# Kernel tuning notes

Hardware: AMD Instinct MI355X
Metric: run time of the kernel (lower is better)

The kernel has to match this reference:

```python
import jax, jax.numpy as jnp
import numpy as np

B, C_IN, C_OUT, N_VERT, K = 8, 64, 64, 40962, 7


def setup_inputs() -> dict:
    key = jax.random.key(0)
    k1, k2, k3, k4 = jax.random.split(key, 4)
    x = jax.random.normal(k1, (B, C_IN, N_VERT), dtype=jnp.float32)
    neigh_indices = jax.random.randint(k2, (N_VERT, K), 0, N_VERT, dtype=jnp.int64)
    # nn.Linear(in=K*C_IN, out=C_OUT): weight [C_OUT, K*C_IN], bias [C_OUT]
    W = jax.random.normal(k3, (C_OUT, C_IN * K), dtype=jnp.float32) * (1.0 / np.sqrt(C_IN * K))
    b = jax.random.normal(k4, (C_OUT,), dtype=jnp.float32) * 0.01
    return {"x": x, "neigh_indices": neigh_indices, "W": W, "b": b}


def reference(x, neigh_indices, W, b):
    # x: [B, C_in, N]; neigh_indices: [N, K]
    # gather neighbor features: [B, C_in, N, K]
    gathered = x[:, :, neigh_indices]
    # Linear over flattened (C_in, K) per vertex. The torch flatten order is
    # (c, k) since mat is [B, N, C_in, K] reshaped to [B*N, C_in*K].
    Wr = W.reshape(W.shape[0], x.shape[1], neigh_indices.shape[1])  # [C_out, C_in, K]
    out = jnp.einsum('bcnk,ock->bon', gathered, Wr) + b[None, :, None]
    return out  # [B, C_out, N]
```

## Files before the change

### kernel.cpp

```cpp
#include <hip/hip_runtime.h>

#define BB 8
#define CI 64
#define CO 64
#define NV 40962
#define KN 7
#define KKD 448

typedef unsigned short u16;
typedef unsigned int u32;

typedef __bf16 bf16x8 __attribute__((ext_vector_type(8)));
typedef float f32x16 __attribute__((ext_vector_type(16)));

__device__ inline u16 f2bf(float f) {
    u32 u = __builtin_bit_cast(u32, f);
    u32 r = (u + 0x7FFFu + ((u >> 16) & 1u)) >> 16;
    return (u16)r;
}

__device__ inline void gload_lds16(const void* g, void* l) {
    __builtin_amdgcn_global_load_lds(
        (const __attribute__((address_space(1))) u32*)g,
        (__attribute__((address_space(3))) u32*)l, 16, 0, 0);
}

__global__ void transpose_x(const float* __restrict__ x, u16* __restrict__ xT) {
    __shared__ u16 tile[64][72];
    const int b = blockIdx.y;
    const int n0 = blockIdx.x * 64;
    const int tid = threadIdx.x;

#pragma unroll
    for (int i = 0; i < 16; ++i) {
        int flat = i * 256 + tid;
        int c = flat >> 6;
        int nn = flat & 63;
        int n = n0 + nn;
        if (n < NV) {
            float v = __builtin_nontemporal_load(&x[((size_t)b * CI + c) * NV + n]);
            tile[nn][c] = f2bf(v);
        }
    }
    __syncthreads();

#pragma unroll
    for (int i = 0; i < 2; ++i) {
        int flat8 = i * 256 + tid;
        int nn = flat8 >> 3;
        int c0 = (flat8 & 7) * 8;
        int n = n0 + nn;
        if (n < NV) {
            uint4 v = *(const uint4*)&tile[nn][c0];
            *(uint4*)&xT[((size_t)b * NV + n) * CI + c0] = v;
        }
    }
}

__global__ void pack_w(const float* __restrict__ W, u16* __restrict__ Wf) {
    int e = blockIdx.x * 256 + threadIdx.x;
    if (e < 2 * 28 * 64 * 8) {
        int j = e & 7;
        int lane = (e >> 3) & 63;
        int sg = e >> 9;
        int s = sg % 28;
        int rg = sg / 28;
        int o = rg * 32 + (lane & 31);
        int kk = s * 16 + ((lane >> 5) << 3) + j;
        int kn = kk >> 6;
        int c = kk & 63;
        Wf[e] = f2bf(W[o * KKD + c * KN + kn]);
    }
}

__global__ __launch_bounds__(256, 6) void conv_mfma(
    const u16* __restrict__ xT, const u16* __restrict__ Wf,
    const int* __restrict__ idx, const float* __restrict__ bias,
    float* __restrict__ out) {
    __shared__ alignas(16) u16 G[3][4096];

    const int bid = blockIdx.x;
    const int b = bid & 7;
    const int n0 = (bid >> 3) * 64;
    const int t = threadIdx.x;
    const int lane = t & 63;
    const int w = t >> 6;
    const int rg = w & 1;
    const int cg = w >> 1;
    const int col = lane & 31;
    const int half = lane >> 5;

    const char* xbc = (const char*)(xT + (size_t)b * NV * CI);
    const char* wfc = (const char*)Wf;

    const int sr0 = t >> 3;
    const int q = t & 7;
    const int qe = q ^ (sr0 & 7);

    int g0 = n0 + sr0;        if (g0 >= NV) g0 = NV - 1;
    int g1 = n0 + 32 + sr0;   if (g1 >= NV) g1 = NV - 1;

    int j0[KN], j1[KN];
    {
        int4 lo0 = *(const int4*)(idx + (size_t)g0 * KN);
        int4 hi0 = *(const int4*)(idx + (size_t)g0 * KN + 3);
        int4 lo1 = *(const int4*)(idx + (size_t)g1 * KN);
        int4 hi1 = *(const int4*)(idx + (size_t)g1 * KN + 3);
        j0[0] = lo0.x; j0[1] = lo0.y; j0[2] = lo0.z; j0[3] = lo0.w;
        j0[4] = hi0.y; j0[5] = hi0.z; j0[6] = hi0.w;
        j1[0] = lo1.x; j1[1] = lo1.y; j1[2] = lo1.z; j1[3] = lo1.w;
        j1[4] = hi1.y; j1[5] = hi1.z; j1[6] = hi1.w;
    }

    char* gb = (char*)&G[0][0];
    const u32 dst0 = (u32)(w * 1024);
    const u32 dst1 = (u32)(4096 + w * 1024);

    const int brow = cg * 32 + col;
    const u32 rbase = (u32)(brow * 128);
    const u32 rmask = (u32)(brow & 7) << 4;

    const u32 abase = (u32)((rg * 28) * 1024 + lane * 16);

    f32x16 acc{};

    gload_lds16(xbc + (size_t)j0[0] * 128 + qe * 16, gb + 0 * 8192 + dst0);
    gload_lds16(xbc + (size_t)j1[0] * 128 + qe * 16, gb + 0 * 8192 + dst1);
    __builtin_amdgcn_sched_barrier(0);
    uint4 acur0 = *(const uint4*)(wfc + abase + 0 * 1024);
    uint4 acur1 = *(const uint4*)(wfc + abase + 1 * 1024);
    uint4 acur2 = *(const uint4*)(wfc + abase + 2 * 1024);
    uint4 acur3 = *(const uint4*)(wfc + abase + 3 * 1024);
    __builtin_amdgcn_sched_barrier(0);
    gload_lds16(xbc + (size_t)j0[1] * 128 + qe * 16, gb + 1 * 8192 + dst0);
    gload_lds16(xbc + (size_t)j1[1] * 128 + qe * 16, gb + 1 * 8192 + dst1);
    __builtin_amdgcn_sched_barrier(0);

#pragma unroll
    for (int k = 0; k < KN; ++k) {
        uint4 an0, an1, an2, an3;
        if (k + 1 < KN) {
            u32 ab = abase + (u32)((k + 1) * 4 * 1024);
            an0 = *(const uint4*)(wfc + ab + 0 * 1024);
            an1 = *(const uint4*)(wfc + ab + 1 * 1024);
            an2 = *(const uint4*)(wfc + ab + 2 * 1024);
            an3 = *(const uint4*)(wfc + ab + 3 * 1024);
        }
        __builtin_amdgcn_sched_barrier(0);

        if (k <= 5) asm volatile("s_waitcnt vmcnt(6)" ::: "memory");
        else        asm volatile("s_waitcnt vmcnt(0)" ::: "memory");
        __builtin_amdgcn_sched_barrier(0);
        __builtin_amdgcn_s_barrier();
        __builtin_amdgcn_sched_barrier(0);

        if (k + 2 < KN) {
            u32 db = (u32)(((k + 2) % 3) * 8192);
            gload_lds16(xbc + (size_t)j0[k + 2] * 128 + qe * 16, gb + db + dst0);
            gload_lds16(xbc + (size_t)j1[k + 2] * 128 + qe * 16, gb + db + dst1);
        }
        __builtin_amdgcn_sched_barrier(0);

        const char* gsrc = gb + (u32)((k % 3) * 8192);
#pragma unroll
        for (int sub = 0; sub < 4; ++sub) {
            u32 boff = rbase + ((((u32)sub * 32) + (u32)half * 16) ^ rmask);
            uint4 bf = *(const uint4*)(gsrc + boff);
            uint4 af = (sub == 0) ? acur0 : (sub == 1) ? acur1 : (sub == 2) ? acur2 : acur3;
            acc = __builtin_amdgcn_mfma_f32_32x32x16_bf16(
                __builtin_bit_cast(bf16x8, af),
                __builtin_bit_cast(bf16x8, bf), acc, 0, 0, 0);
        }

        if (k + 1 < KN) { acur0 = an0; acur1 = an1; acur2 = an2; acur3 = an3; }
    }

    const int v = n0 + cg * 32 + col;
    if (v < NV) {
        float* ob = out + (size_t)b * CO * NV + v;
#pragma unroll
        for (int r = 0; r < 16; ++r) {
            int rowo = (r & 3) + 8 * (r >> 2) + 4 * half;
            int o = rg * 32 + rowo;
            ob[(size_t)o * NV] = acc[r] + bias[o];
        }
    }
}

__global__ void naive_conv(const float* __restrict__ x, const int* __restrict__ idx,
                           const float* __restrict__ W, const float* __restrict__ bias,
                           float* __restrict__ out) {
    const int b = blockIdx.y;
    const int n = blockIdx.x * 4 + (threadIdx.x & 3);
    const int o = threadIdx.x >> 2;
    if (n >= NV) return;
    float acc = bias[o];
    const float* xb = x + (size_t)b * CI * NV;
    const float* wo = W + o * KKD;
    for (int k = 0; k < KN; ++k) {
        int j = idx[n * KN + k];
        for (int c = 0; c < CI; ++c)
            acc += xb[(size_t)c * NV + j] * wo[c * KN + k];
    }
    out[((size_t)b * CO + o) * NV + n] = acc;
}

extern "C" void kernel_launch(void* const* d_in, const int* in_sizes, int n_in,
                              void* d_out, int out_size, void* d_ws, size_t ws_size,
                              hipStream_t stream) {
    const float* x    = (const float*)d_in[0];
    const int*   idx  = (const int*)d_in[1];
    const float* W    = (const float*)d_in[2];
    const float* bias = (const float*)d_in[3];
    float* out = (float*)d_out;

    const size_t xT_bytes = (size_t)BB * NV * CI * 2;
    const size_t wf_bytes = (size_t)2 * 28 * 64 * 8 * 2;
    const size_t need = xT_bytes + wf_bytes;

    if (ws_size >= need) {
        u16* xT = (u16*)d_ws;
        u16* Wf = (u16*)((char*)d_ws + xT_bytes);
        transpose_x<<<dim3((NV + 63) / 64, BB), 256, 0, stream>>>(x, xT);
        pack_w<<<dim3(112), 256, 0, stream>>>(W, Wf);
        const int ntiles = (NV + 63) / 64;
        conv_mfma<<<dim3(ntiles * BB), 256, 0, stream>>>(xT, Wf, idx, bias, out);
    } else {
        naive_conv<<<dim3((NV + 3) / 4, BB), 256, 0, stream>>>(x, idx, W, bias, out);
    }
}
```

Before: 79.34 us.

## Make conv kernel persistent with register-resident weights and cross-tile gather prefetch

The MFMA conv kernel becomes persistent: a grid of 512 blocks loops over vertex tiles with a stride of 64 tiles. Each wave loads its full packed weight slice into registers once and caches the bias. The 3-slot LDS ring now runs across tile boundaries, so gathers for the next tile's first neighbours and its index loads are issued during the current tile's compute. The aim is to remove per-block setup, reloading of weights, and the pipeline drain at tile ends. The cost is heavier register use and lower occupancy (launch bounds 2), and only 512 blocks may underfill the GPU's compute units.

```diff
diff --git a/kernel.cpp b/kernel.cpp
--- a/kernel.cpp
+++ b/kernel.cpp
@@ -6,12 +6,16 @@
 #define NV 40962
 #define KN 7
 #define KKD 448
+#define NTILES 641
+#define BPB 64
 
 typedef unsigned short u16;
 typedef unsigned int u32;
 
 typedef __bf16 bf16x8 __attribute__((ext_vector_type(8)));
 typedef float f32x16 __attribute__((ext_vector_type(16)));
+
+#define WAITV(N) asm volatile("s_waitcnt vmcnt(" #N ")" ::: "memory")
 
 __device__ inline u16 f2bf(float f) {
     u32 u = __builtin_bit_cast(u32, f);
@@ -73,7 +77,7 @@
     }
 }
 
-__global__ __launch_bounds__(256, 6) void conv_mfma(
+__global__ __launch_bounds__(256, 2) void conv_mfma(
     const u16* __restrict__ xT, const u16* __restrict__ Wf,
     const int* __restrict__ idx, const float* __restrict__ bias,
     float* __restrict__ out) {
@@ -81,7 +85,7 @@
 
     const int bid = blockIdx.x;
     const int b = bid & 7;
-    const int n0 = (bid >> 3) * 64;
+    const int tile0 = bid >> 3;
     const int t = threadIdx.x;
     const int lane = t & 63;
     const int w = t >> 6;
@@ -92,27 +96,11 @@
 
     const char* xbc = (const char*)(xT + (size_t)b * NV * CI);
     const char* wfc = (const char*)Wf;
+    char* gb = (char*)&G[0][0];
 
     const int sr0 = t >> 3;
     const int q = t & 7;
-    const int qe = q ^ (sr0 & 7);
-
-    int g0 = n0 + sr0;        if (g0 >= NV) g0 = NV - 1;
-    int g1 = n0 + 32 + sr0;   if (g1 >= NV) g1 = NV - 1;
-
-    int j0[KN], j1[KN];
-    {
-        int4 lo0 = *(const int4*)(idx + (size_t)g0 * KN);
-        int4 hi0 = *(const int4*)(idx + (size_t)g0 * KN + 3);
-        int4 lo1 = *(const int4*)(idx + (size_t)g1 * KN);
-        int4 hi1 = *(const int4*)(idx + (size_t)g1 * KN + 3);
-        j0[0] = lo0.x; j0[1] = lo0.y; j0[2] = lo0.z; j0[3] = lo0.w;
-        j0[4] = hi0.y; j0[5] = hi0.z; j0[6] = hi0.w;
-        j1[0] = lo1.x; j1[1] = lo1.y; j1[2] = lo1.z; j1[3] = lo1.w;
-        j1[4] = hi1.y; j1[5] = hi1.z; j1[6] = hi1.w;
-    }
-
-    char* gb = (char*)&G[0][0];
+    const u32 qe16 = (u32)((q ^ (sr0 & 7)) << 4);
     const u32 dst0 = (u32)(w * 1024);
     const u32 dst1 = (u32)(4096 + w * 1024);
 
@@ -120,70 +108,118 @@
     const u32 rbase = (u32)(brow * 128);
     const u32 rmask = (u32)(brow & 7) << 4;
 
-    const u32 abase = (u32)((rg * 28) * 1024 + lane * 16);
-
-    f32x16 acc{};
-
-    gload_lds16(xbc + (size_t)j0[0] * 128 + qe * 16, gb + 0 * 8192 + dst0);
-    gload_lds16(xbc + (size_t)j1[0] * 128 + qe * 16, gb + 0 * 8192 + dst1);
+    int jc0[KN], jc1[KN], jn0[KN], jn1[KN];
+    {
+        int nn0 = tile0 * 64 + sr0;      if (nn0 >= NV) nn0 = NV - 1;
+        int nn1 = tile0 * 64 + 32 + sr0; if (nn1 >= NV) nn1 = NV - 1;
+        int4 lo0 = *(const int4*)(idx + (size_t)nn0 * KN);
+        int4 hi0 = *(const int4*)(idx + (size_t)nn0 * KN + 3);
+        int4 lo1 = *(const int4*)(idx + (size_t)nn1 * KN);
+        int4 hi1 = *(const int4*)(idx + (size_t)nn1 * KN + 3);
+        jc0[0]=lo0.x; jc0[1]=lo0.y; jc0[2]=lo0.z; jc0[3]=lo0.w;
+        jc0[4]=hi0.y; jc0[5]=hi0.z; jc0[6]=hi0.w;
+        jc1[0]=lo1.x; jc1[1]=lo1.y; jc1[2]=lo1.z; jc1[3]=lo1.w;
+        jc1[4]=hi1.y; jc1[5]=hi1.z; jc1[6]=hi1.w;
+    }
+    float bv[16];
+#pragma unroll
+    for (int r = 0; r < 16; ++r) {
+        int rowo = (r & 3) + 8 * (r >> 2) + 4 * half;
+        bv[r] = bias[rg * 32 + rowo];
+    }
+    uint4 A[28];
+#pragma unroll
+    for (int s = 0; s < 28; ++s)
+        A[s] = *(const uint4*)(wfc + (u32)((rg * 28 + s) * 1024) + (u32)(lane * 16));
     __builtin_amdgcn_sched_barrier(0);
-    uint4 acur0 = *(const uint4*)(wfc + abase + 0 * 1024);
-    uint4 acur1 = *(const uint4*)(wfc + abase + 1 * 1024);
-    uint4 acur2 = *(const uint4*)(wfc + abase + 2 * 1024);
-    uint4 acur3 = *(const uint4*)(wfc + abase + 3 * 1024);
+    gload_lds16(xbc + (size_t)jc0[0] * 128 + qe16, gb + 0 * 8192 + dst0);
+    gload_lds16(xbc + (size_t)jc1[0] * 128 + qe16, gb + 0 * 8192 + dst1);
+    gload_lds16(xbc + (size_t)jc0[1] * 128 + qe16, gb + 1 * 8192 + dst0);
+    gload_lds16(xbc + (size_t)jc1[1] * 128 + qe16, gb + 1 * 8192 + dst1);
     __builtin_amdgcn_sched_barrier(0);
-    gload_lds16(xbc + (size_t)j0[1] * 128 + qe * 16, gb + 1 * 8192 + dst0);
-    gload_lds16(xbc + (size_t)j1[1] * 128 + qe * 16, gb + 1 * 8192 + dst1);
-    __builtin_amdgcn_sched_barrier(0);
-
-#pragma unroll
-    for (int k = 0; k < KN; ++k) {
-        uint4 an0, an1, an2, an3;
-        if (k + 1 < KN) {
-            u32 ab = abase + (u32)((k + 1) * 4 * 1024);
-            an0 = *(const uint4*)(wfc + ab + 0 * 1024);
-            an1 = *(const uint4*)(wfc + ab + 1 * 1024);
-            an2 = *(const uint4*)(wfc + ab + 2 * 1024);
-            an3 = *(const uint4*)(wfc + ab + 3 * 1024);
-        }
-        __builtin_amdgcn_sched_barrier(0);
-
-        if (k <= 5) asm volatile("s_waitcnt vmcnt(6)" ::: "memory");
-        else        asm volatile("s_waitcnt vmcnt(0)" ::: "memory");
-        __builtin_amdgcn_sched_barrier(0);
-        __builtin_amdgcn_s_barrier();
-        __builtin_amdgcn_sched_barrier(0);
-
-        if (k + 2 < KN) {
-            u32 db = (u32)(((k + 2) % 3) * 8192);
-            gload_lds16(xbc + (size_t)j0[k + 2] * 128 + qe * 16, gb + db + dst0);
-            gload_lds16(xbc + (size_t)j1[k + 2] * 128 + qe * 16, gb + db + dst1);
-        }
-        __builtin_amdgcn_sched_barrier(0);
-
-        const char* gsrc = gb + (u32)((k % 3) * 8192);
-#pragma unroll
-        for (int sub = 0; sub < 4; ++sub) {
-            u32 boff = rbase + ((((u32)sub * 32) + (u32)half * 16) ^ rmask);
-            uint4 bf = *(const uint4*)(gsrc + boff);
-            uint4 af = (sub == 0) ? acur0 : (sub == 1) ? acur1 : (sub == 2) ? acur2 : acur3;
-            acc = __builtin_amdgcn_mfma_f32_32x32x16_bf16(
-                __builtin_bit_cast(bf16x8, af),
-                __builtin_bit_cast(bf16x8, bf), acc, 0, 0, 0);
-        }
-
-        if (k + 1 < KN) { acur0 = an0; acur1 = an1; acur2 = an2; acur3 = an3; }
-    }
-
-    const int v = n0 + cg * 32 + col;
-    if (v < NV) {
-        float* ob = out + (size_t)b * CO * NV + v;
-#pragma unroll
-        for (int r = 0; r < 16; ++r) {
-            int rowo = (r & 3) + 8 * (r >> 2) + 4 * half;
-            int o = rg * 32 + rowo;
-            ob[(size_t)o * NV] = acc[r] + bias[o];
-        }
+
+    f32x16 acc;
+#pragma unroll
+    for (int i = 0; i < 16; ++i) acc[i] = 0.f;
+
+    int tcur = tile0;
+    int ring = 0;
+    bool first = true;
+
+    while (true) {
+        const int n0 = tcur * 64;
+        int tnxt = tcur + BPB;
+        const bool last = (tnxt >= NTILES);
+        if (last) tnxt = tcur;
+
+#pragma unroll
+        for (int k = 0; k < KN; ++k) {
+            if (k == 0)      { if (first) WAITV(2);  else WAITV(18); }
+            else if (k == 1) { if (first) WAITV(6);  else WAITV(22); }
+            else if (k == 2) WAITV(6);
+            else             WAITV(2);
+            __builtin_amdgcn_sched_barrier(0);
+            __builtin_amdgcn_s_barrier();
+            __builtin_amdgcn_sched_barrier(0);
+
+            {
+                int slot = ring + ((k + 2) % 3); if (slot >= 3) slot -= 3;
+                char* d = gb + (u32)slot * 8192u;
+                if (k <= 4) {
+                    gload_lds16(xbc + (size_t)jc0[k + 2] * 128 + qe16, d + dst0);
+                    gload_lds16(xbc + (size_t)jc1[k + 2] * 128 + qe16, d + dst1);
+                } else {
+                    gload_lds16(xbc + (size_t)jn0[k - 5] * 128 + qe16, d + dst0);
+                    gload_lds16(xbc + (size_t)jn1[k - 5] * 128 + qe16, d + dst1);
+                }
+            }
+            if (k == 0) {
+                int nn0 = tnxt * 64 + sr0;      if (nn0 >= NV) nn0 = NV - 1;
+                int nn1 = tnxt * 64 + 32 + sr0; if (nn1 >= NV) nn1 = NV - 1;
+                int4 lo0 = *(const int4*)(idx + (size_t)nn0 * KN);
+                int4 hi0 = *(const int4*)(idx + (size_t)nn0 * KN + 3);
+                int4 lo1 = *(const int4*)(idx + (size_t)nn1 * KN);
+                int4 hi1 = *(const int4*)(idx + (size_t)nn1 * KN + 3);
+                jn0[0]=lo0.x; jn0[1]=lo0.y; jn0[2]=lo0.z; jn0[3]=lo0.w;
+                jn0[4]=hi0.y; jn0[5]=hi0.z; jn0[6]=hi0.w;
+                jn1[0]=lo1.x; jn1[1]=lo1.y; jn1[2]=lo1.z; jn1[3]=lo1.w;
+                jn1[4]=hi1.y; jn1[5]=hi1.z; jn1[6]=hi1.w;
+            }
+            __builtin_amdgcn_sched_barrier(0);
+
+            {
+                int slot = ring + (k % 3); if (slot >= 3) slot -= 3;
+                const char* gsrc = gb + (u32)slot * 8192u;
+#pragma unroll
+                for (int s = 0; s < 4; ++s) {
+                    u32 boff = rbase + ((((u32)s * 32) + (u32)half * 16) ^ rmask);
+                    uint4 bf = *(const uint4*)(gsrc + boff);
+                    acc = __builtin_amdgcn_mfma_f32_32x32x16_bf16(
+                        __builtin_bit_cast(bf16x8, A[k * 4 + s]),
+                        __builtin_bit_cast(bf16x8, bf), acc, 0, 0, 0);
+                }
+            }
+        }
+
+        {
+            const int v = n0 + cg * 32 + col;
+            if (v < NV) {
+                float* ob = out + (size_t)b * CO * NV + v;
+#pragma unroll
+                for (int r = 0; r < 16; ++r) {
+                    int rowo = (r & 3) + 8 * (r >> 2) + 4 * half;
+                    ob[(size_t)(rg * 32 + rowo) * NV] = acc[r] + bv[r];
+                }
+            }
+        }
+        if (last) break;
+#pragma unroll
+        for (int i = 0; i < KN; ++i) { jc0[i] = jn0[i]; jc1[i] = jn1[i]; }
+#pragma unroll
+        for (int i = 0; i < 16; ++i) acc[i] = 0.f;
+        tcur = tnxt;
+        ring = ring + 1; if (ring >= 3) ring = 0;
+        first = false;
     }
 }
 
@@ -223,8 +259,7 @@
         u16* Wf = (u16*)((char*)d_ws + xT_bytes);
         transpose_x<<<dim3((NV + 63) / 64, BB), 256, 0, stream>>>(x, xT);
         pack_w<<<dim3(112), 256, 0, stream>>>(W, Wf);
-        const int ntiles = (NV + 63) / 64;
-        conv_mfma<<<dim3(ntiles * BB), 256, 0, stream>>>(xT, Wf, idx, bias, out);
+        conv_mfma<<<dim3(8 * BPB), 256, 0, stream>>>(xT, Wf, idx, bias, out);
     } else {
         naive_conv<<<dim3((NV + 3) / 4, BB), 256, 0, stream>>>(x, idx, W, bias, out);
     }
```

New measurement: 82.67 us. 4.2% more time.
